# Kernel optimization log

Measured on AMD Instinct MI355X. Metric: run time of the kernel, lower is better.

## Reference

```python
import jax, jax.numpy as jnp
import numpy as np
import math

HEAD_DIM = 128
N_HEADS = 32
HIDDEN = 4096
ROPE_THETA = 10000.0
NEG = -100000.0


def _rope_cos_sin(pos):
    # pos: [B, L] int -> cos, sin: [B, L, HEAD_DIM]
    inv_freq = 1.0 / (ROPE_THETA ** (jnp.arange(0, HEAD_DIM, 2, dtype=jnp.float32) / HEAD_DIM))
    freqs = pos.astype(jnp.float32)[..., None] * inv_freq  # [B, L, HEAD_DIM//2]
    emb = jnp.concatenate([freqs, freqs], axis=-1)
    return jnp.cos(emb), jnp.sin(emb)


def _rotate_half(x):
    x1, x2 = x[..., : HEAD_DIM // 2], x[..., HEAD_DIM // 2 :]
    return jnp.concatenate([-x2, x1], axis=-1)


def _apply_rope(h, cos, sin):
    # h: [B, H, L, D], cos/sin: [B, L, D] -> unsqueeze head dim
    return h * cos[:, None] + _rotate_half(h) * sin[:, None]


def setup_inputs() -> dict:
    key = jax.random.key(0)
    ks = jax.random.split(key, 8)
    B, Q, K = 2, 1024, 2048
    inp = {
        "hidden_states": jax.random.normal(ks[0], (B, Q, HIDDEN), jnp.float32),
        "key_value_states": jax.random.normal(ks[1], (B, K, HIDDEN), jnp.float32),
        "Wq": jax.random.normal(ks[2], (HIDDEN, HIDDEN), jnp.float32) * 0.02,
        "Wk": jax.random.normal(ks[3], (HIDDEN, HIDDEN), jnp.float32) * 0.02,
        "Wv": jax.random.normal(ks[4], (HIDDEN, HIDDEN), jnp.float32) * 0.02,
        "Wo": jax.random.normal(ks[5], (HIDDEN, HIDDEN), jnp.float32) * 0.02,
        "position_ids": jnp.arange(B * Q, dtype=jnp.int32).reshape(B, Q),
        "text_position_ids": jnp.arange(B * K, dtype=jnp.int32).reshape(B, K),
        "simul_mask_idx": jnp.sort(jax.random.randint(ks[6], (B, Q), 0, K, jnp.int32), axis=-1),
        "window_size": jax.random.randint(ks[7], (B, Q), 0, 512, jnp.int32),
    }
    return inp


def reference(hidden_states, key_value_states, Wq, Wk, Wv, Wo,
              position_ids, text_position_ids, simul_mask_idx, window_size):
    B, Qlen, _ = hidden_states.shape
    Klen = key_value_states.shape[1]

    q = jnp.einsum('bqh,hd->bqd', hidden_states, Wq.T).reshape(B, Qlen, N_HEADS, HEAD_DIM).transpose(0, 2, 1, 3)
    k = jnp.einsum('bkh,hd->bkd', key_value_states, Wk.T).reshape(B, Klen, N_HEADS, HEAD_DIM).transpose(0, 2, 1, 3)
    v = jnp.einsum('bkh,hd->bkd', key_value_states, Wv.T).reshape(B, Klen, N_HEADS, HEAD_DIM).transpose(0, 2, 1, 3)

    cos, sin = _rope_cos_sin(position_ids)
    q = _apply_rope(q, cos, sin)
    t_cos, t_sin = _rope_cos_sin(text_position_ids)
    k = _apply_rope(k, t_cos, t_sin)

    scores = jnp.einsum('bhqd,bhkd->bhqk', q, k) / math.sqrt(HEAD_DIM)

    # simul windowed mask: key j visible for query i iff clamp(idx-w,0) <= j < idx
    idx = simul_mask_idx[:, None, :, None]          # [B,1,Q,1]
    w = window_size[:, None, :, None]               # [B,1,Q,1]
    tmp = jnp.arange(Klen, dtype=jnp.int32)         # [K]
    mask = (jnp.clip(idx - w, 0) <= tmp) & (tmp < idx)  # [B,1,Q,K]
    scores = jnp.where(mask, scores, NEG)

    probs = jax.nn.softmax(scores.astype(jnp.float32), axis=-1).astype(q.dtype)
    attn = jnp.einsum('bhqk,bhkd->bhqd', probs, v)
    attn = attn.transpose(0, 2, 1, 3).reshape(B, Qlen, HIDDEN)
    out = jnp.einsum('bqh,hd->bqd', attn, Wo.T)
    return out
```

## Files before the change

### kernel.cpp

```cpp
#include <hip/hip_runtime.h>
#include <stdint.h>

#define BATCH 2
#define QLEN 1024
#define KLEN 2048
#define NH 32
#define HD 128
#define HID 4096

typedef short bf16x8 __attribute__((ext_vector_type(8)));
typedef float f32x4 __attribute__((ext_vector_type(4)));
typedef float f32x16 __attribute__((ext_vector_type(16)));
typedef unsigned short u16;

typedef const __attribute__((address_space(1))) void gvoid;
typedef __attribute__((address_space(3))) void lvoid;

__device__ __forceinline__ u16 f2bf(float f) {
  union { float f; uint32_t u; } x; x.f = f;
  uint32_t r = x.u + 0x7fffu + ((x.u >> 16) & 1u);
  return (u16)(r >> 16);
}
__device__ __forceinline__ float bf2f(u16 h) {
  union { uint32_t u; float f; } x; x.u = ((uint32_t)h) << 16;
  return x.f;
}
__device__ __forceinline__ f32x4 mfma16(bf16x8 a, bf16x8 b, f32x4 c) {
  return __builtin_amdgcn_mfma_f32_16x16x32_bf16(a, b, c, 0, 0, 0);
}
__device__ __forceinline__ f32x16 mfma32(bf16x8 a, bf16x8 b, f32x16 c) {
  return __builtin_amdgcn_mfma_f32_32x32x16_bf16(a, b, c, 0, 0, 0);
}
__device__ __forceinline__ void glds16(const u16* src, char* dst) {
  __builtin_amdgcn_global_load_lds((gvoid*)src, (lvoid*)dst, 16, 0, 0);
}

__device__ __forceinline__ void cvt8(const float* in, u16* out, int i) {
  const float4* p = (const float4*)(in + i);
  float4 a = p[0], b = p[1];
  union { u16 h[8]; bf16x8 v; } u;
  u.h[0] = f2bf(a.x); u.h[1] = f2bf(a.y); u.h[2] = f2bf(a.z); u.h[3] = f2bf(a.w);
  u.h[4] = f2bf(b.x); u.h[5] = f2bf(b.y); u.h[6] = f2bf(b.z); u.h[7] = f2bf(b.w);
  *(bf16x8*)(out + i) = u.v;
}

__global__ __launch_bounds__(256) void cvt_all_kernel(
    const float* __restrict__ hs, u16* __restrict__ hid_b,
    const float* __restrict__ kvs, u16* __restrict__ kv_b,
    const float* __restrict__ Wk, u16* __restrict__ w1,
    const float* __restrict__ Wv, u16* __restrict__ w2,
    const float* __restrict__ Wq, u16* __restrict__ w3,
    const float* __restrict__ Wo, u16* __restrict__ w4) {
  int bid = blockIdx.x;
  const float* src;
  u16* dst;
  int base;
  if (bid < 4096) { src = hs; dst = hid_b; base = bid; }
  else if (bid < 12288) { src = kvs; dst = kv_b; base = bid - 4096; }
  else if (bid < 20480) { src = Wk; dst = w1; base = bid - 12288; }
  else if (bid < 28672) { src = Wv; dst = w2; base = bid - 20480; }
  else if (bid < 36864) { src = Wq; dst = w3; base = bid - 28672; }
  else { src = Wo; dst = w4; base = bid - 36864; }
  cvt8(src, dst, base * 2048 + threadIdx.x * 8);
}

#define RD_A32(CB, ks, PS, mf) \
  (*(const bf16x8*)(lds + (CB) + (ks) * 16384 + (mf) * 2048 + rAb + (PS)))
#define RD_B32(CB, ks, PS, nf) \
  (*(const bf16x8*)(lds + 65536 + (CB) + (ks) * 16384 + (nf) * 2048 + rBb + (PS)))

#define MFMA_CLUSTER32()                                                         \
    __builtin_amdgcn_s_barrier();                                                \
    asm volatile("s_waitcnt lgkmcnt(0)" ::: "memory");                           \
    __builtin_amdgcn_sched_barrier(0);                                           \
    __builtin_amdgcn_s_setprio(1);                                               \
    _Pragma("unroll") for (int mf = 0; mf < 4; mf++)                             \
      _Pragma("unroll") for (int nf = 0; nf < 2; nf++)                           \
        acc[mf][nf] = mfma32(af[mf], bfv[nf], acc[mf][nf]);                      \
    __builtin_amdgcn_s_setprio(0);                                               \
    __builtin_amdgcn_s_barrier();

#define TILE32(CB, NB, K0N)                                                      \
  {                                                                              \
    bf16x8 af[4], bfv[2];                                                        \
    _Pragma("unroll") for (int x = 0; x < 4; x++) af[x] = RD_A32(CB, 0, ps0, x); \
    _Pragma("unroll") for (int x = 0; x < 2; x++) bfv[x] = RD_B32(CB, 0, ps0, x);\
    glds16(As0 + (K0N), dA + (NB));                                              \
    glds16(As1 + (K0N), dA + (NB) + 8192);                                       \
    MFMA_CLUSTER32()                                                             \
    _Pragma("unroll") for (int x = 0; x < 4; x++) af[x] = RD_A32(CB, 0, ps1, x); \
    _Pragma("unroll") for (int x = 0; x < 2; x++) bfv[x] = RD_B32(CB, 0, ps1, x);\
    glds16(Bs0 + (K0N), dB + (NB));                                              \
    glds16(Bs1 + (K0N), dB + (NB) + 8192);                                       \
    asm volatile("s_waitcnt vmcnt(4)" ::: "memory");                             \
    MFMA_CLUSTER32()                                                             \
    _Pragma("unroll") for (int x = 0; x < 4; x++) af[x] = RD_A32(CB, 1, ps0, x); \
    _Pragma("unroll") for (int x = 0; x < 2; x++) bfv[x] = RD_B32(CB, 1, ps0, x);\
    glds16(As0 + (K0N) + 32, dA + (NB) + 16384);                                 \
    glds16(As1 + (K0N) + 32, dA + (NB) + 16384 + 8192);                          \
    MFMA_CLUSTER32()                                                             \
    _Pragma("unroll") for (int x = 0; x < 4; x++) af[x] = RD_A32(CB, 1, ps1, x); \
    _Pragma("unroll") for (int x = 0; x < 2; x++) bfv[x] = RD_B32(CB, 1, ps1, x);\
    glds16(Bs0 + (K0N) + 32, dB + (NB) + 16384);                                 \
    glds16(Bs1 + (K0N) + 32, dB + (NB) + 16384 + 8192);                          \
    asm volatile("s_waitcnt vmcnt(4)" ::: "memory");                             \
    MFMA_CLUSTER32()                                                             \
  }

template <int EPI>
__global__ __launch_bounds__(512, 2) void gemm256(const u16* __restrict__ A,
                                                  const u16* __restrict__ Bw,
                                                  void* __restrict__ Cout,
                                                  int M, int N, int K) {
  (void)M;
  __shared__ alignas(16) char lds[131072];
  const int tid = threadIdx.x;
  const int lane = tid & 63, wv = tid >> 6;
  const int wvm = wv >> 2, wvn = wv & 3;
  const int l31 = lane & 31, hi2 = lane >> 5;

  const int gx = gridDim.x;
  const int nwg = gx * gridDim.y;
  const int lin = blockIdx.y * gx + blockIdx.x;
  const int swz = (lin & 7) * (nwg >> 3) + (lin >> 3);
  const int m0 = (swz / gx) * 256, n0 = (swz % gx) * 256;

  const int srow = tid >> 2;
  const int sg = (tid & 3) ^ ((srow >> 1) & 3);
  const u16* As0 = A + (size_t)(m0 + srow) * K + sg * 8;
  const u16* As1 = A + (size_t)(m0 + 128 + srow) * K + sg * 8;
  const u16* Bs0 = Bw + (size_t)(n0 + srow) * K + sg * 8;
  const u16* Bs1 = Bw + (size_t)(n0 + 128 + srow) * K + sg * 8;
  char* dA = lds + tid * 16;
  char* dB = lds + 65536 + tid * 16;

  const int xorv = (l31 >> 1) & 3;
  const int ps0 = (hi2 ^ xorv) << 4;
  const int ps1 = ((2 + hi2) ^ xorv) << 4;
  const int rAb = (wvm * 128 + l31) * 64;
  const int rBb = (wvn * 64 + l31) * 64;

  f32x16 acc[4][2];
#pragma unroll
  for (int mf = 0; mf < 4; mf++)
#pragma unroll
    for (int nf = 0; nf < 2; nf++)
#pragma unroll
      for (int e = 0; e < 16; e++) acc[mf][nf][e] = 0.f;

  glds16(As0, dA);
  glds16(As1, dA + 8192);
  glds16(Bs0, dB);
  glds16(Bs1, dB + 8192);
  glds16(As0 + 32, dA + 16384);
  glds16(As1 + 32, dA + 16384 + 8192);
  glds16(Bs0 + 32, dB + 16384);
  glds16(Bs1 + 32, dB + 16384 + 8192);
  asm volatile("s_waitcnt vmcnt(4)" ::: "memory");
  __builtin_amdgcn_s_barrier();

  const int NT = K >> 6;
  for (int t = 0; t < NT; t += 2) {
    const int kA = (t + 1) * 64;
    TILE32(0, 32768, kA)
    const int kB = (((t + 2) < NT) ? (t + 2) : 0) * 64;
    TILE32(32768, 0, kB)
  }

  if (EPI == 2) {
    u16* C = (u16*)Cout;
#pragma unroll
    for (int mf = 0; mf < 4; mf++) {
      int rowf = m0 + wvm * 128 + mf * 32 + 4 * hi2;
#pragma unroll
      for (int nf = 0; nf < 2; nf++) {
        int col = n0 + wvn * 64 + nf * 32 + l31;
#pragma unroll
        for (int q = 0; q < 4; q++)
#pragma unroll
          for (int j = 0; j < 4; j++)
            C[(size_t)(rowf + q * 8 + j) * N + col] = f2bf(acc[mf][nf][q * 4 + j]);
      }
    }
  } else {
    u16* C = (u16*)Cout;
#pragma unroll
    for (int mf = 0; mf < 4; mf++) {
      int rowf = m0 + wvm * 128 + mf * 32 + 4 * hi2;
#pragma unroll
      for (int nf = 0; nf < 2; nf++) {
        int col = n0 + wvn * 64 + nf * 32 + l31;
#pragma unroll
        for (int q = 0; q < 4; q++) {
          int rowb = rowf + q * 8;
          int bb = rowb >> 11, tt = rowb & 2047;
          uint64_t pk = (uint64_t)f2bf(acc[mf][nf][q * 4]) |
                        ((uint64_t)f2bf(acc[mf][nf][q * 4 + 1]) << 16) |
                        ((uint64_t)f2bf(acc[mf][nf][q * 4 + 2]) << 32) |
                        ((uint64_t)f2bf(acc[mf][nf][q * 4 + 3]) << 48);
          *(uint64_t*)(C + ((size_t)(bb * 4096 + col)) * 2048 + tt) = pk;
        }
      }
    }
  }
}

#define RD_AT(BUF, ks, mf) \
  (*(const bf16x8*)(lds + (BUF) * 32768 + (ks) * 16384 + (mf) * 1024 + rA))
#define RD_BT(BUF, ks, nf) \
  (*(const bf16x8*)(lds + 98304 + (BUF) * 16384 + (ks) * 8192 + (nf) * 1024 + rB))

#define STG_H0(BUF, K0N)                                    \
  glds16(AsT0 + (K0N), dAT + (BUF) * 32768);                \
  glds16(AsT1 + (K0N), dAT + (BUF) * 32768 + 8192);         \
  glds16(BsT0 + (K0N), dBT + (BUF) * 16384);

#define STG_H1(BUF, K0N)                                    \
  glds16(AsT0 + (K0N) + 32, dAT + (BUF) * 32768 + 16384);   \
  glds16(AsT1 + (K0N) + 32, dAT + (BUF) * 32768 + 16384 + 8192); \
  glds16(BsT0 + (K0N) + 32, dBT + (BUF) * 16384 + 8192);

#define TILE256T(CUR, STG, K0N)                                                  \
  {                                                                              \
    bf16x8 af[4], bfr[4];                                                        \
    _Pragma("unroll") for (int x = 0; x < 4; x++) af[x] = RD_AT(CUR, 0, x);      \
    _Pragma("unroll") for (int x = 0; x < 4; x++) bfr[x] = RD_BT(CUR, 0, x);     \
    STG_H0(STG, K0N)                                                             \
    __builtin_amdgcn_s_barrier();                                                \
    asm volatile("s_waitcnt lgkmcnt(0)" ::: "memory");                           \
    __builtin_amdgcn_sched_barrier(0);                                           \
    __builtin_amdgcn_s_setprio(1);                                               \
    _Pragma("unroll") for (int mf = 0; mf < 4; mf++)                             \
      _Pragma("unroll") for (int nf = 0; nf < 4; nf++)                           \
        acc[mf][nf] = mfma16(af[mf], bfr[nf], acc[mf][nf]);                      \
    __builtin_amdgcn_s_setprio(0);                                               \
    __builtin_amdgcn_s_barrier();                                                \
    _Pragma("unroll") for (int x = 0; x < 4; x++) af[x] = RD_AT(CUR, 1, x);      \
    _Pragma("unroll") for (int x = 0; x < 4; x++) bfr[x] = RD_BT(CUR, 1, x);     \
    STG_H1(STG, K0N)                                                             \
    asm volatile("s_waitcnt vmcnt(6)" ::: "memory");                             \
    __builtin_amdgcn_s_barrier();                                                \
    asm volatile("s_waitcnt lgkmcnt(0)" ::: "memory");                           \
    __builtin_amdgcn_sched_barrier(0);                                           \
    __builtin_amdgcn_s_setprio(1);                                               \
    _Pragma("unroll") for (int mf = 0; mf < 4; mf++)                             \
      _Pragma("unroll") for (int nf = 0; nf < 4; nf++)                           \
        acc[mf][nf] = mfma16(af[mf], bfr[nf], acc[mf][nf]);                      \
    __builtin_amdgcn_s_setprio(0);                                               \
    __builtin_amdgcn_s_barrier();                                                \
  }

template <int EPI>
__global__ __launch_bounds__(512, 2) void gemm256T(const u16* __restrict__ W,
                                                   const u16* __restrict__ Act,
                                                   void* __restrict__ Cout) {
  const int K = HID;
  __shared__ alignas(16) char lds[147456];
  const int tid = threadIdx.x;
  const int lane = tid & 63, wv = tid >> 6;
  const int wvm = wv >> 1, wvn = wv & 1;
  const int g = lane >> 4, l16 = lane & 15;

  const int lin = blockIdx.y * 16 + blockIdx.x;
  const int swz = (lin & 7) * 32 + (lin >> 3);
  const int m0 = (swz >> 4) * 256;
  const int n0 = (swz & 15) * 128;

  const int srow = tid >> 2;
  const int sg = (tid & 3) ^ ((srow >> 1) & 3);
  const u16* AsT0 = W + (size_t)(m0 + srow) * K + sg * 8;
  const u16* AsT1 = W + (size_t)(m0 + 128 + srow) * K + sg * 8;
  const u16* BsT0 = Act + (size_t)(n0 + srow) * K + sg * 8;
  char* dAT = lds + tid * 16;
  char* dBT = lds + 98304 + tid * 16;

  const int rsw = (g ^ ((l16 >> 1) & 3)) << 4;
  const int rA = (wvm * 64 + l16) * 64 + rsw;
  const int rB = (wvn * 64 + l16) * 64 + rsw;

  f32x4 acc[4][4];
#pragma unroll
  for (int mf = 0; mf < 4; mf++)
#pragma unroll
    for (int nf = 0; nf < 4; nf++) acc[mf][nf] = (f32x4){0.f, 0.f, 0.f, 0.f};

  STG_H0(0, 0)
  STG_H1(0, 0)
  STG_H0(1, 64)
  STG_H1(1, 64)
  asm volatile("s_waitcnt vmcnt(6)" ::: "memory");
  __builtin_amdgcn_s_barrier();

  for (int t = 0; t < 63; t += 3) {
    const int k1 = (t + 2) * 64;
    const int k2 = (t + 3) * 64;
    const int k3 = ((t + 4) < 64) ? (t + 4) * 64 : 0;
    TILE256T(0, 2, k1)
    TILE256T(1, 0, k2)
    TILE256T(2, 1, k3)
  }
  {
    bf16x8 af[4], bfr[4];
#pragma unroll
    for (int x = 0; x < 4; x++) af[x] = RD_AT(0, 0, x);
#pragma unroll
    for (int x = 0; x < 4; x++) bfr[x] = RD_BT(0, 0, x);
#pragma unroll
    for (int mf = 0; mf < 4; mf++)
#pragma unroll
      for (int nf = 0; nf < 4; nf++)
        acc[mf][nf] = mfma16(af[mf], bfr[nf], acc[mf][nf]);
#pragma unroll
    for (int x = 0; x < 4; x++) af[x] = RD_AT(0, 1, x);
#pragma unroll
    for (int x = 0; x < 4; x++) bfr[x] = RD_BT(0, 1, x);
#pragma unroll
    for (int mf = 0; mf < 4; mf++)
#pragma unroll
      for (int nf = 0; nf < 4; nf++)
        acc[mf][nf] = mfma16(af[mf], bfr[nf], acc[mf][nf]);
  }

  if (EPI == 0) {
    float* C = (float*)Cout;
#pragma unroll
    for (int mf = 0; mf < 4; mf++) {
      int frow = m0 + wvm * 64 + mf * 16 + g * 4;
#pragma unroll
      for (int nf = 0; nf < 4; nf++) {
        int col = n0 + wvn * 64 + nf * 16 + l16;
        float4 v = {acc[mf][nf][0], acc[mf][nf][1], acc[mf][nf][2], acc[mf][nf][3]};
        *(float4*)(C + (size_t)col * HID + frow) = v;
      }
    }
  } else {
    u16* C = (u16*)Cout;
#pragma unroll
    for (int mf = 0; mf < 4; mf++) {
      int frow = m0 + wvm * 64 + mf * 16 + g * 4;
#pragma unroll
      for (int nf = 0; nf < 4; nf++) {
        int col = n0 + wvn * 64 + nf * 16 + l16;
        uint64_t pk = (uint64_t)f2bf(acc[mf][nf][0]) |
                      ((uint64_t)f2bf(acc[mf][nf][1]) << 16) |
                      ((uint64_t)f2bf(acc[mf][nf][2]) << 32) |
                      ((uint64_t)f2bf(acc[mf][nf][3]) << 48);
        *(uint64_t*)(C + (size_t)col * HID + frow) = pk;
      }
    }
  }
}

__device__ __forceinline__ void rope_row(const u16* x, float p, u16* out,
                                         int rowsPerB, int row, int t) {
  int b = row / rowsPerB, r = row - b * rowsPerB;
  int h = t >> 3, i0 = (t & 7) * 8;
  const u16* xr = x + (size_t)row * HID + h * HD;
  bf16x8 lov = *(const bf16x8*)(xr + i0);
  bf16x8 hiv = *(const bf16x8*)(xr + 64 + i0);
  union { u16 h[8]; bf16x8 v; } olo, ohi;
#pragma unroll
  for (int j = 0; j < 8; j++) {
    float lo = bf2f((u16)lov[j]);
    float hi = bf2f((u16)hiv[j]);
    float f = exp2f(-(float)(i0 + j) * (13.287712379549449f / 64.0f));
    float ang = p * f;
    float s, c;
    sincosf(ang, &s, &c);
    olo.h[j] = f2bf(lo * c - hi * s);
    ohi.h[j] = f2bf(hi * c + lo * s);
  }
  u16* ob = out + ((size_t)((b * NH + h) * rowsPerB) + r) * HD;
  *(bf16x8*)(ob + i0) = olo.v;
  *(bf16x8*)(ob + 64 + i0) = ohi.v;
}

__global__ __launch_bounds__(256) void rope_vmean_kernel(
    const u16* __restrict__ qsrc, const u16* __restrict__ ksrc,
    u16* __restrict__ qdst, u16* __restrict__ kdst,
    const int* __restrict__ pos, const int* __restrict__ tpos,
    const u16* __restrict__ vt, float* __restrict__ vm) {
  int bid = blockIdx.x;
  if (bid >= 6144) {
    int row = (bid - 6144) * 4 + (threadIdx.x >> 6);
    int lane = threadIdx.x & 63;
    const u16* p = vt + (size_t)row * KLEN;
    float s = 0.f;
#pragma unroll
    for (int it = 0; it < 4; it++) {
      bf16x8 v = *(const bf16x8*)(p + it * 512 + lane * 8);
#pragma unroll
      for (int j = 0; j < 8; j++) s += bf2f((u16)v[j]);
    }
    for (int off = 32; off; off >>= 1) s += __shfl_xor(s, off);
    if (lane == 0) vm[row] = s * (1.0f / (float)KLEN);
    return;
  }
  if (bid < 2048) {
    rope_row(qsrc, (float)pos[bid], qdst, QLEN, bid, threadIdx.x);
  } else {
    int row = bid - 2048;
    rope_row(ksrc, (float)tpos[row], kdst, KLEN, row, threadIdx.x);
  }
}

__global__ __launch_bounds__(256, 2) void attn_kernel(
    const u16* __restrict__ qb, const u16* __restrict__ kb,
    const u16* __restrict__ vt, const float* __restrict__ vm,
    const int* __restrict__ idxA, const int* __restrict__ wA,
    u16* __restrict__ aout) {
  __shared__ u16 Ks[32][136];
  __shared__ u16 Vs[128][40];
  __shared__ u16 Ps[4][16][40];
  __shared__ int sS[64], sE[64], sRange[2];

  const int tid = threadIdx.x, lane = tid & 63, wv = tid >> 6;
  const int g = lane >> 4, l16 = lane & 15;
  const int blk = blockIdx.x;
  const int qt = blk & 15, bh = blk >> 4, b = bh >> 5, h = bh & 31;
  const int q0 = qt * 64;
  const float SCALE = 0.08838834764831845f;

  if (tid < 64) {
    int e = idxA[b * QLEN + q0 + tid];
    int w = wA[b * QLEN + q0 + tid];
    int s = e - w;
    if (s < 0) s = 0;
    sS[tid] = s;
    sE[tid] = e;
  }
  __syncthreads();
  if (wv == 0) {
    int s_ = sS[lane], e_ = sE[lane];
    int mn = (e_ > s_) ? s_ : 0x7fffffff;
    int mx = (e_ > s_) ? e_ : 0;
    for (int off = 32; off; off >>= 1) {
      mn = min(mn, __shfl_xor(mn, off));
      mx = max(mx, __shfl_xor(mx, off));
    }
    if (lane == 0) { sRange[0] = mn; sRange[1] = mx; }
  }
  __syncthreads();
  const int klo = sRange[0], khi = sRange[1];

  int rs[4], re[4];
#pragma unroll
  for (int r = 0; r < 4; r++) {
    rs[r] = sS[wv * 16 + g * 4 + r];
    re[r] = sE[wv * 16 + g * 4 + r];
  }

  bf16x8 qf[4];
  {
    const u16* qp = qb + ((size_t)(bh * QLEN + q0 + wv * 16 + l16)) * HD + g * 8;
#pragma unroll
    for (int s4 = 0; s4 < 4; s4++) qf[s4] = *(const bf16x8*)(qp + s4 * 32);
  }

  f32x4 acc[8];
#pragma unroll
  for (int db = 0; db < 8; db++) acc[db] = (f32x4){0.f, 0.f, 0.f, 0.f};
  float mrow[4] = {-1e30f, -1e30f, -1e30f, -1e30f};
  float lsum[4] = {0.f, 0.f, 0.f, 0.f};

  if (klo < khi) {
    for (int t0 = (klo & ~31); t0 < khi; t0 += 32) {
      {
        int idx = tid * 8;
        int kr = idx >> 7, kc = idx & 127;
        *(bf16x8*)(&Ks[kr][kc]) =
            *(const bf16x8*)(kb + ((size_t)(bh * KLEN + t0 + kr)) * HD + kc);
        int kr2 = kr + 16;
        *(bf16x8*)(&Ks[kr2][kc]) =
            *(const bf16x8*)(kb + ((size_t)(bh * KLEN + t0 + kr2)) * HD + kc);
        int vr = idx >> 5, vc = idx & 31;
        *(bf16x8*)(&Vs[vr][vc]) =
            *(const bf16x8*)(vt + ((size_t)(bh * HD + vr)) * KLEN + t0 + vc);
        int vr2 = vr + 64;
        *(bf16x8*)(&Vs[vr2][vc]) =
            *(const bf16x8*)(vt + ((size_t)(bh * HD + vr2)) * KLEN + t0 + vc);
      }
      __syncthreads();

      f32x4 sc0 = (f32x4){0.f, 0.f, 0.f, 0.f};
      f32x4 sc1 = (f32x4){0.f, 0.f, 0.f, 0.f};
#pragma unroll
      for (int s4 = 0; s4 < 4; s4++) {
        bf16x8 k0 = *(const bf16x8*)(&Ks[l16][s4 * 32 + g * 8]);
        bf16x8 k1 = *(const bf16x8*)(&Ks[16 + l16][s4 * 32 + g * 8]);
        sc0 = mfma16(qf[s4], k0, sc0);
        sc1 = mfma16(qf[s4], k1, sc1);
      }

      float resc[4];
#pragma unroll
      for (int r = 0; r < 4; r++) {
        float v0 = sc0[r] * SCALE, v1 = sc1[r] * SCALE;
        int t_0 = t0 + l16, t_1 = t0 + 16 + l16;
        v0 = (t_0 >= rs[r] && t_0 < re[r]) ? v0 : -1e30f;
        v1 = (t_1 >= rs[r] && t_1 < re[r]) ? v1 : -1e30f;
        float mx = fmaxf(v0, v1);
        mx = fmaxf(mx, __shfl_xor(mx, 1));
        mx = fmaxf(mx, __shfl_xor(mx, 2));
        mx = fmaxf(mx, __shfl_xor(mx, 4));
        mx = fmaxf(mx, __shfl_xor(mx, 8));
        float mn = fmaxf(mrow[r], mx);
        float rc = __expf(mrow[r] - mn);
        float p0 = __expf(v0 - mn), p1 = __expf(v1 - mn);
        mrow[r] = mn;
        resc[r] = rc;
        float ps = p0 + p1;
        ps += __shfl_xor(ps, 1);
        ps += __shfl_xor(ps, 2);
        ps += __shfl_xor(ps, 4);
        ps += __shfl_xor(ps, 8);
        lsum[r] = lsum[r] * rc + ps;
        Ps[wv][g * 4 + r][l16] = f2bf(p0);
        Ps[wv][g * 4 + r][16 + l16] = f2bf(p1);
      }
#pragma unroll
      for (int db = 0; db < 8; db++) {
#pragma unroll
        for (int r = 0; r < 4; r++) acc[db][r] *= resc[r];
      }
      bf16x8 pf = *(const bf16x8*)(&Ps[wv][l16][g * 8]);
#pragma unroll
      for (int db = 0; db < 8; db++) {
        bf16x8 vf = *(const bf16x8*)(&Vs[db * 16 + l16][g * 8]);
        acc[db] = mfma16(pf, vf, acc[db]);
      }
      __syncthreads();
    }
  }

#pragma unroll
  for (int r = 0; r < 4; r++) {
    int lr = wv * 16 + g * 4 + r;
    int q = q0 + lr;
    bool empty = (re[r] <= rs[r]);
    float inv = empty ? 0.f : 1.0f / lsum[r];
    u16* orow = aout + ((size_t)(b * QLEN + q)) * HID + h * HD;
#pragma unroll
    for (int db = 0; db < 8; db++) {
      float o = empty ? vm[bh * HD + db * 16 + l16] : acc[db][r] * inv;
      orow[db * 16 + l16] = f2bf(o);
    }
  }
}

extern "C" void kernel_launch(void* const* d_in, const int* in_sizes, int n_in,
                              void* d_out, int out_size, void* d_ws, size_t ws_size,
                              hipStream_t stream) {
  (void)in_sizes; (void)n_in; (void)out_size; (void)ws_size;
  const float* hs = (const float*)d_in[0];
  const float* kvs = (const float*)d_in[1];
  const float* Wq = (const float*)d_in[2];
  const float* Wk = (const float*)d_in[3];
  const float* Wv = (const float*)d_in[4];
  const float* Wo = (const float*)d_in[5];
  const int* pos = (const int*)d_in[6];
  const int* tpos = (const int*)d_in[7];
  const int* sidx = (const int*)d_in[8];
  const int* wsz = (const int*)d_in[9];
  float* out = (float*)d_out;

  char* ws = (char*)d_ws;
  size_t off = 0;
  auto alloc = [&](size_t bytes) -> void* {
    void* p = ws + off;
    off += (bytes + 255) & ~(size_t)255;
    return p;
  };
  const size_t WN = (size_t)HID * HID;
  const size_t NQ = (size_t)BATCH * QLEN * HID;
  const size_t NK = (size_t)BATCH * KLEN * HID;

  u16* w1 = (u16*)alloc(WN * 2);
  u16* w2 = (u16*)alloc(WN * 2);
  u16* w3 = (u16*)alloc(WN * 2);
  u16* w4 = (u16*)alloc(WN * 2);
  u16* hid_b = (u16*)alloc(NQ * 2);
  u16* kv_b = (u16*)alloc(NK * 2);
  u16* sc_b = (u16*)alloc(NK * 2);
  u16* qp_b = (u16*)alloc(NQ * 2);
  u16* q_b = (u16*)alloc(NQ * 2);
  u16* k_b = (u16*)alloc(NK * 2);
  u16* vt_b = (u16*)alloc(NK * 2);
  float* vmean = (float*)alloc((size_t)BATCH * NH * HD * 4);

  cvt_all_kernel<<<45056, 256, 0, stream>>>(hs, hid_b, kvs, kv_b, Wk, w1,
                                            Wv, w2, Wq, w3, Wo, w4);
  gemm256<2><<<dim3(16, 16), 512, 0, stream>>>(kv_b, w1, sc_b,
                                               BATCH * KLEN, HID, HID);
  gemm256<1><<<dim3(16, 16), 512, 0, stream>>>(kv_b, w2, vt_b,
                                               BATCH * KLEN, HID, HID);
  gemm256T<2><<<dim3(16, 16), 512, 0, stream>>>(w3, hid_b, qp_b);

  rope_vmean_kernel<<<8192, 256, 0, stream>>>(qp_b, sc_b, q_b, k_b, pos, tpos,
                                              vt_b, vmean);

  attn_kernel<<<BATCH * NH * (QLEN / 64), 256, 0, stream>>>(
      q_b, k_b, vt_b, vmean, sidx, wsz, sc_b);

  gemm256T<0><<<dim3(16, 16), 512, 0, stream>>>(w4, sc_b, out);
}
```

Before: 620.5 us.

## Split weight conversion into per-GEMM passes reusing one buffer; tweak LDS swizzle

```diff
diff --git a/kernel.cpp b/kernel.cpp
--- a/kernel.cpp
+++ b/kernel.cpp
@@ -44,24 +44,24 @@
   *(bf16x8*)(out + i) = u.v;
 }
 
-__global__ __launch_bounds__(256) void cvt_all_kernel(
-    const float* __restrict__ hs, u16* __restrict__ hid_b,
-    const float* __restrict__ kvs, u16* __restrict__ kv_b,
-    const float* __restrict__ Wk, u16* __restrict__ w1,
-    const float* __restrict__ Wv, u16* __restrict__ w2,
-    const float* __restrict__ Wq, u16* __restrict__ w3,
-    const float* __restrict__ Wo, u16* __restrict__ w4) {
-  int bid = blockIdx.x;
-  const float* src;
-  u16* dst;
-  int base;
-  if (bid < 4096) { src = hs; dst = hid_b; base = bid; }
-  else if (bid < 12288) { src = kvs; dst = kv_b; base = bid - 4096; }
-  else if (bid < 20480) { src = Wk; dst = w1; base = bid - 12288; }
-  else if (bid < 28672) { src = Wv; dst = w2; base = bid - 20480; }
-  else if (bid < 36864) { src = Wq; dst = w3; base = bid - 28672; }
-  else { src = Wo; dst = w4; base = bid - 36864; }
-  cvt8(src, dst, base * 2048 + threadIdx.x * 8);
+__global__ __launch_bounds__(256) void cvt_kernel(const float* __restrict__ in,
+                                                  u16* __restrict__ out, int n) {
+  int i = (blockIdx.x * 256 + threadIdx.x) * 8;
+  if (i >= n) return;
+  cvt8(in, out, i);
+}
+
+__global__ __launch_bounds__(256) void cvt2_kernel(const float* __restrict__ s0,
+                                                   u16* __restrict__ d0, int n0,
+                                                   const float* __restrict__ s1,
+                                                   u16* __restrict__ d1, int n1) {
+  int i = (blockIdx.x * 256 + threadIdx.x) * 8;
+  if (i < n0) {
+    cvt8(s0, d0, i);
+  } else {
+    int j = i - n0;
+    if (j < n1) cvt8(s1, d1, j);
+  }
 }
 
 #define RD_A32(CB, ks, PS, mf) \
@@ -126,7 +126,7 @@
   const int m0 = (swz / gx) * 256, n0 = (swz % gx) * 256;
 
   const int srow = tid >> 2;
-  const int sg = (tid & 3) ^ ((srow >> 1) & 3);
+  const int sg = (tid & 3) ^ ((srow >> 1) & 3) ^ ((srow >> 4) & 1);
   const u16* As0 = A + (size_t)(m0 + srow) * K + sg * 8;
   const u16* As1 = A + (size_t)(m0 + 128 + srow) * K + sg * 8;
   const u16* Bs0 = Bw + (size_t)(n0 + srow) * K + sg * 8;
@@ -134,7 +134,7 @@
   char* dA = lds + tid * 16;
   char* dB = lds + 65536 + tid * 16;
 
-  const int xorv = (l31 >> 1) & 3;
+  const int xorv = ((l31 >> 1) & 3) ^ ((l31 >> 4) & 1);
   const int ps0 = (hi2 ^ xorv) << 4;
   const int ps1 = ((2 + hi2) ^ xorv) << 4;
   const int rAb = (wvm * 128 + l31) * 64;
@@ -577,8 +577,6 @@
 
   u16* w1 = (u16*)alloc(WN * 2);
   u16* w2 = (u16*)alloc(WN * 2);
-  u16* w3 = (u16*)alloc(WN * 2);
-  u16* w4 = (u16*)alloc(WN * 2);
   u16* hid_b = (u16*)alloc(NQ * 2);
   u16* kv_b = (u16*)alloc(NK * 2);
   u16* sc_b = (u16*)alloc(NK * 2);
@@ -588,13 +586,16 @@
   u16* vt_b = (u16*)alloc(NK * 2);
   float* vmean = (float*)alloc((size_t)BATCH * NH * HD * 4);
 
-  cvt_all_kernel<<<45056, 256, 0, stream>>>(hs, hid_b, kvs, kv_b, Wk, w1,
-                                            Wv, w2, Wq, w3, Wo, w4);
+  cvt2_kernel<<<(int)((NQ + NK) / 2048), 256, 0, stream>>>(hs, hid_b, (int)NQ,
+                                                           kvs, kv_b, (int)NK);
+  cvt2_kernel<<<(int)(2 * WN / 2048), 256, 0, stream>>>(Wk, w1, (int)WN,
+                                                        Wv, w2, (int)WN);
   gemm256<2><<<dim3(16, 16), 512, 0, stream>>>(kv_b, w1, sc_b,
                                                BATCH * KLEN, HID, HID);
   gemm256<1><<<dim3(16, 16), 512, 0, stream>>>(kv_b, w2, vt_b,
                                                BATCH * KLEN, HID, HID);
-  gemm256T<2><<<dim3(16, 16), 512, 0, stream>>>(w3, hid_b, qp_b);
+  cvt_kernel<<<(int)(WN / 2048), 256, 0, stream>>>(Wq, w1, (int)WN);
+  gemm256T<2><<<dim3(16, 16), 512, 0, stream>>>(w1, hid_b, qp_b);
 
   rope_vmean_kernel<<<8192, 256, 0, stream>>>(qp_b, sc_b, q_b, k_b, pos, tpos,
                                               vt_b, vmean);
@@ -602,5 +603,6 @@
   attn_kernel<<<BATCH * NH * (QLEN / 64), 256, 0, stream>>>(
       q_b, k_b, vt_b, vmean, sidx, wsz, sc_b);
 
-  gemm256T<0><<<dim3(16, 16), 512, 0, stream>>>(w4, sc_b, out);
-}
+  cvt_kernel<<<(int)(WN / 2048), 256, 0, stream>>>(Wo, w1, (int)WN);
+  gemm256T<0><<<dim3(16, 16), 512, 0, stream>>>(w1, sc_b, out);
+}
```

After: 583.2 us. 6.0% less time.
